# Kernel tuning notes

Measured on AMD Instinct MI355X. Metric: run time of the kernel, lower is better.

The kernel has to match this reference:

```python
import jax, jax.numpy as jnp
import numpy as np

H = 50  # hidden size hard-coded in the torch module


def _lstm_layer(x, W_ih, W_hh, b_ih, b_hh):
    """x: [B, T, D_in] -> outputs [B, T, H]. PyTorch gate order: i, f, g, o."""
    B = x.shape[0]
    # precompute input projection for all timesteps: [B, T, 4H]
    x_proj = jnp.einsum('btd,gd->btg', x, W_ih) + b_ih + b_hh
    x_proj = jnp.swapaxes(x_proj, 0, 1)  # time-major [T, B, 4H]

    def step(carry, xt):
        h, c = carry
        gates = xt + h @ W_hh.T  # [B, 4H]
        i, f, g, o = jnp.split(gates, 4, axis=-1)
        c = jax.nn.sigmoid(f) * c + jax.nn.sigmoid(i) * jnp.tanh(g)
        h = jax.nn.sigmoid(o) * jnp.tanh(c)
        return (h, c), h

    h0 = jnp.zeros((B, H), dtype=x.dtype)
    c0 = jnp.zeros((B, H), dtype=x.dtype)
    (_, _), hs = jax.lax.scan(step, (h0, c0), x_proj)
    return jnp.swapaxes(hs, 0, 1)  # [B, T, H]


def setup_inputs() -> dict:
    key = jax.random.key(0)
    ks = jax.random.split(key, 11)
    B, T = 4096, 512
    s = 1.0 / np.sqrt(H)  # torch LSTM init scale
    return {
        'x': jax.random.normal(ks[0], (B, T, 1), dtype=jnp.float32),
        'W_ih0': jax.random.normal(ks[1], (4 * H, 1), dtype=jnp.float32) * s,
        'W_hh0': jax.random.normal(ks[2], (4 * H, H), dtype=jnp.float32) * s,
        'b_ih0': jax.random.normal(ks[3], (4 * H,), dtype=jnp.float32) * s,
        'b_hh0': jax.random.normal(ks[4], (4 * H,), dtype=jnp.float32) * s,
        'W_ih1': jax.random.normal(ks[5], (4 * H, H), dtype=jnp.float32) * s,
        'W_hh1': jax.random.normal(ks[6], (4 * H, H), dtype=jnp.float32) * s,
        'b_ih1': jax.random.normal(ks[7], (4 * H,), dtype=jnp.float32) * s,
        'b_hh1': jax.random.normal(ks[8], (4 * H,), dtype=jnp.float32) * s,
        'W_fc': jax.random.normal(ks[9], (1, H), dtype=jnp.float32) * s,
        'b_fc': jax.random.normal(ks[10], (1,), dtype=jnp.float32) * s,
    }


def reference(x, W_ih0, W_hh0, b_ih0, b_hh0, W_ih1, W_hh1, b_ih1, b_hh1, W_fc, b_fc):
    h1 = _lstm_layer(x, W_ih0, W_hh0, b_ih0, b_hh0)   # [B, T, H]
    h2 = _lstm_layer(h1, W_ih1, W_hh1, b_ih1, b_hh1)  # [B, T, H]
    last = h2[:, -1, :]                                # [B, H]
    return last @ W_fc.T + b_fc                        # [B, 1]
```

## Files before the change

kernel.cpp:

```cpp
#include <hip/hip_runtime.h>


#define TT 512
#define HH 50
#define BT 16
#define NTHR 1024
#define L2E 1.44269504f

typedef _Float16 half8 __attribute__((ext_vector_type(8)));
typedef float floatx4 __attribute__((ext_vector_type(4)));

static __device__ __forceinline__ float fexp2(float x) { return __builtin_amdgcn_exp2f(x); }
static __device__ __forceinline__ float frcp(float x)  { return __builtin_amdgcn_rcpf(x); }

static __device__ __forceinline__ float cell_update(float gi, float gf, float gg,
                                                    float go, float& c) {
    float Ei = fexp2(gi);
    float Eg = fexp2(gg);
    float Ef = fexp2(gf);
    float Eo = fexp2(go);
    float p1 = (1.0f + Ei) * (1.0f + Eg);
    float fe = 1.0f + Ef;
    float R  = frcp(fe * p1);
    c = R * (c * p1 + (1.0f - Eg) * fe);
    float cl = fminf(fmaxf(c, -18.0f), 18.0f);
    float Ec = fexp2(cl * (-2.0f * L2E));
    float Ro = frcp((1.0f + Eo) * (1.0f + Ec));
    return (1.0f - Ec) * Ro;
}

#define MFMA(a, b, c) __builtin_amdgcn_mfma_f32_16x16x32_f16((a), (b), (c), 0, 0, 0)

template<int NJ, bool XW>
static __device__ __forceinline__ void run_l0(
    int tbase, int ln, _Float16 (*H1)[1024], const float* xs,
    const float* __restrict__ W_ih0, const float* __restrict__ W_hh0,
    const float* __restrict__ b_ih0, const float* __restrict__ b_hh0)
{
    const int m = ln & 15, q = ln >> 4;
    const float GSC[4] = { -L2E, -L2E, -2.0f * L2E, -L2E };

    half8 a0[NJ][2];
    float c[NJ];
    int   widx[NJ];
#pragma unroll
    for (int j = 0; j < NJ; ++j) {
        const int  tau  = tbase + j;
        const int  uA   = 4 * tau + (m >> 2);
        const int  gA   = m & 3;
        const bool rokA = (uA < HH);
        const int  wrow = gA * HH + uA;
        const float sA  = GSC[gA];
#pragma unroll
        for (int ks = 0; ks < 2; ++ks) {
            half8 h8;
#pragma unroll
            for (int jj = 0; jj < 8; ++jj) {
                int k = ks * 32 + q * 8 + jj;
                float w = 0.f;
                if (rokA) {
                    if (k < HH)       w = W_hh0[wrow * HH + k];
                    else if (k == 50) w = b_ih0[wrow] + b_hh0[wrow];
                    else if (k == 51) w = W_ih0[wrow];
                }
                h8[jj] = (_Float16)(sA * w);
            }
            a0[j][ks] = h8;
        }
        const int uC = 4 * tau + q;
        const int kh = (uC < HH) ? uC : (uC + 2);
        widx[j] = ((kh >> 5) * 64 + ((kh >> 3) & 3) * 16 + m) * 8 + (kh & 7);
        c[j] = 0.f;
    }

    __syncthreads();

    {
        const float xv = xs[m];
#pragma unroll
        for (int j = 0; j < NJ; ++j) {
            const int  uC = 4 * (tbase + j) + q;
            const bool vC = (uC < HH);
            float g4[4];
#pragma unroll
            for (int g = 0; g < 4; ++g) {
                int rg = g * HH + (vC ? uC : 0);
                g4[g] = vC ? GSC[g] * ((b_ih0[rg] + b_hh0[rg]) + W_ih0[rg] * xv) : 0.f;
            }
            float h = cell_update(g4[0], g4[1], g4[2], g4[3], c[j]);
            H1[0][widx[j]] = (_Float16)h;
        }
    }
    __syncthreads();

    const floatx4 ZERO = { 0.f, 0.f, 0.f, 0.f };
    for (int s = 1; s <= 513; ++s) {
        if (s <= 511) {
            const _Float16* bufR = H1[(s - 1) & 3];
            _Float16*       bufW = H1[s & 3];
            if (XW) {
                if (ln < 16)
                    bufW[(96 + ln) * 8 + 3] = (_Float16)xs[(s + 1) * BT + ln];
            }
            half8 b0 = *(const half8*)&bufR[(0  + ln) * 8];
            half8 b1 = *(const half8*)&bufR[(64 + ln) * 8];
#pragma unroll
            for (int j = 0; j < NJ; ++j) {
                floatx4 a = MFMA(a0[j][0], b0, ZERO);
                a = MFMA(a0[j][1], b1, a);
                float h = cell_update(a[0], a[1], a[2], a[3], c[j]);
                bufW[widx[j]] = (_Float16)h;
            }
        }
        __syncthreads();
    }
}

template<int NJ>
static __device__ __forceinline__ void run_l1(
    int tbase, int ln, _Float16 (*H1)[1024], _Float16 (*H2)[1024],
    const float* __restrict__ W_ih1, const float* __restrict__ W_hh1,
    const float* __restrict__ b_ih1, const float* __restrict__ b_hh1)
{
    const int m = ln & 15, q = ln >> 4;
    const float GSC[4] = { -L2E, -L2E, -2.0f * L2E, -L2E };

    half8 a1[NJ][4];
    float c[NJ];
    int   widx[NJ];
#pragma unroll
    for (int j = 0; j < NJ; ++j) {
        const int  tau  = tbase + j;
        const int  uA   = 4 * tau + (m >> 2);
        const int  gA   = m & 3;
        const bool rokA = (uA < HH);
        const int  wrow = gA * HH + uA;
        const float sA  = GSC[gA];
#pragma unroll
        for (int ks = 0; ks < 4; ++ks) {
            half8 h8;
#pragma unroll
            for (int jj = 0; jj < 8; ++jj) {
                int k = ks * 32 + q * 8 + jj;
                float w = 0.f;
                if (rokA) {
                    if (k < HH)                      w = W_ih1[wrow * HH + k];
                    else if (k == 50)                w = b_ih1[wrow] + b_hh1[wrow];
                    else if (k >= 64 && k < 64 + HH) w = W_hh1[wrow * HH + (k - 64)];
                }
                h8[jj] = (_Float16)(sA * w);
            }
            a1[j][ks] = h8;
        }
        const int uC = 4 * tau + q;
        const int kh = (uC < HH) ? uC : (uC + 2);
        widx[j] = ((kh >> 5) * 64 + ((kh >> 3) & 3) * 16 + m) * 8 + (kh & 7);
        c[j] = 0.f;
    }

    __syncthreads();
    __syncthreads();

    half8 p0 = {}, p1 = {};
    const floatx4 ZERO = { 0.f, 0.f, 0.f, 0.f };
    for (int s = 1; s <= 513; ++s) {
        if (s >= 2) {
            const _Float16* h2R = H2[(s - 1) & 1];
            _Float16*       h2W = H2[s & 1];
            half8 b2 = *(const half8*)&h2R[(0  + ln) * 8];
            half8 b3 = *(const half8*)&h2R[(64 + ln) * 8];
#pragma unroll
            for (int j = 0; j < NJ; ++j) {
                floatx4 a = MFMA(a1[j][0], p0, ZERO);
                a = MFMA(a1[j][1], p1, a);
                a = MFMA(a1[j][2], b2, a);
                a = MFMA(a1[j][3], b3, a);
                float h = cell_update(a[0], a[1], a[2], a[3], c[j]);
                h2W[widx[j]] = (_Float16)h;
            }
        }
        {
            const _Float16* h1R = H1[(s - 1) & 3];
            p0 = *(const half8*)&h1R[(0  + ln) * 8];
            p1 = *(const half8*)&h1R[(64 + ln) * 8];
        }
        __syncthreads();
    }
}

__global__ __launch_bounds__(NTHR, 4) void lstm_mfma(
    const float* __restrict__ x,
    const float* __restrict__ W_ih0, const float* __restrict__ W_hh0,
    const float* __restrict__ b_ih0, const float* __restrict__ b_hh0,
    const float* __restrict__ W_ih1, const float* __restrict__ W_hh1,
    const float* __restrict__ b_ih1, const float* __restrict__ b_hh1,
    const float* __restrict__ W_fc,  const float* __restrict__ b_fc,
    float* __restrict__ out)
{
    __shared__ __align__(16) _Float16 H1[4][1024];
    __shared__ __align__(16) _Float16 H2[2][1024];
    __shared__ float xs[(TT + 1) * BT];

    const int tid = threadIdx.x;
    const int ln  = tid & 63;
    const int wv  = tid >> 6;
    const int b0g = blockIdx.x * BT;

    for (int i = tid; i < BT * TT; i += NTHR) {
        int b = i & 15, t = i >> 4;
        xs[t * BT + b] = x[(size_t)(b0g + b) * TT + t];
    }
    if (tid < BT) xs[TT * BT + tid] = 0.f;
    for (int i = tid; i < 4 * 1024; i += NTHR) ((_Float16*)H1)[i] = (_Float16)0.f;
    for (int i = tid; i < 2 * 1024; i += NTHR) ((_Float16*)H2)[i] = (_Float16)0.f;
    __syncthreads();
    if (tid < 16) {
#pragma unroll
        for (int r = 0; r < 4; ++r) H1[r][(96 + tid) * 8 + 2] = (_Float16)1.0f;
        H1[0][(96 + tid) * 8 + 3] = (_Float16)xs[BT + tid];
    }

    if (wv < 8) {
        if (wv < 5)
            run_l0<2, false>(2 * wv, ln, H1, xs, W_ih0, W_hh0, b_ih0, b_hh0);
        else if (wv == 6)
            run_l0<1, true>(11, ln, H1, xs, W_ih0, W_hh0, b_ih0, b_hh0);
        else
            run_l0<1, false>(wv == 5 ? 10 : 12, ln, H1, xs,
                             W_ih0, W_hh0, b_ih0, b_hh0);
    } else {
        const int w = wv - 8;
        if (w < 3)
            run_l1<1>(w, ln, H1, H2, W_ih1, W_hh1, b_ih1, b_hh1);
        else
            run_l1<2>(3 + 2 * (w - 3), ln, H1, H2,
                      W_ih1, W_hh1, b_ih1, b_hh1);
    }

    if (tid < BT) {
        float a = b_fc[0];
        for (int u = 0; u < HH; ++u) {
            int idx = ((u >> 5) * 64 + ((u >> 3) & 3) * 16 + tid) * 8 + (u & 7);
            a = fmaf((float)H2[1][idx], W_fc[u], a);
        }
        out[b0g + tid] = a;
    }
}

extern "C" void kernel_launch(void* const* d_in, const int* in_sizes, int n_in,
                              void* d_out, int out_size, void* d_ws, size_t ws_size,
                              hipStream_t stream) {
    const float* x     = (const float*)d_in[0];
    const float* W_ih0 = (const float*)d_in[1];
    const float* W_hh0 = (const float*)d_in[2];
    const float* b_ih0 = (const float*)d_in[3];
    const float* b_hh0 = (const float*)d_in[4];
    const float* W_ih1 = (const float*)d_in[5];
    const float* W_hh1 = (const float*)d_in[6];
    const float* b_ih1 = (const float*)d_in[7];
    const float* b_hh1 = (const float*)d_in[8];
    const float* W_fc  = (const float*)d_in[9];
    const float* b_fc  = (const float*)d_in[10];
    float* out = (float*)d_out;

    dim3 grid(4096 / BT);
    dim3 block(NTHR);
    lstm_mfma<<<grid, block, 0, stream>>>(x, W_ih0, W_hh0, b_ih0, b_hh0,
                                          W_ih1, W_hh1, b_ih1, b_hh1,
                                          W_fc, b_fc, out);
}
```

Baseline: 363.7 us.

## Merge both LSTM layers into shared wavefronts with unified double-buffered state

Replaces the 16-wave split (8 waves for layer 0, 8 for layer 1) with 8 waves that each compute a mix of layer-0 and layer-1 unit groups. Both layers now read from one double-buffered shared state array, where layer 1 at step s consumes layer-0 h from step s-1, and waves on the critical path get raised priority. The intent is to halve the threads per block and barrier participants, balance MFMA and transcendental work per wave, and allow 2 blocks per CU. In exchange each wave carries more per-step work, occupancy changes, and the workload mapping (including a mixed tail tile) becomes harder to verify.

```diff
diff --git a/kernel.cpp b/kernel.cpp
--- a/kernel.cpp
+++ b/kernel.cpp
@@ -4,7 +4,7 @@
 #define TT 512
 #define HH 50
 #define BT 16
-#define NTHR 1024
+#define NTHR 512
 #define L2E 1.44269504f
 
 typedef _Float16 half8 __attribute__((ext_vector_type(8)));
@@ -31,164 +31,189 @@
 
 #define MFMA(a, b, c) __builtin_amdgcn_mfma_f32_16x16x32_f16((a), (b), (c), 0, 0, 0)
 
-template<int NJ, bool XW>
-static __device__ __forceinline__ void run_l0(
-    int tbase, int ln, _Float16 (*H1)[1024], const float* xs,
+static __device__ __forceinline__ int widx_of(int unit, int m) {
+    return ((unit >> 5) * 64 + ((unit >> 3) & 3) * 16 + m) * 8 + (unit & 7);
+}
+
+template<int NL0, int NL1, bool MX, bool XW, bool PRIO>
+static __device__ __forceinline__ void run(
+    int l0base, int l1base, int ln, _Float16 (*HS)[2048], const float* xs,
     const float* __restrict__ W_ih0, const float* __restrict__ W_hh0,
-    const float* __restrict__ b_ih0, const float* __restrict__ b_hh0)
-{
-    const int m = ln & 15, q = ln >> 4;
-    const float GSC[4] = { -L2E, -L2E, -2.0f * L2E, -L2E };
-
-    half8 a0[NJ][2];
-    float c[NJ];
-    int   widx[NJ];
-#pragma unroll
-    for (int j = 0; j < NJ; ++j) {
-        const int  tau  = tbase + j;
-        const int  uA   = 4 * tau + (m >> 2);
-        const int  gA   = m & 3;
-        const bool rokA = (uA < HH);
-        const int  wrow = gA * HH + uA;
-        const float sA  = GSC[gA];
-#pragma unroll
-        for (int ks = 0; ks < 2; ++ks) {
-            half8 h8;
-#pragma unroll
-            for (int jj = 0; jj < 8; ++jj) {
-                int k = ks * 32 + q * 8 + jj;
-                float w = 0.f;
-                if (rokA) {
-                    if (k < HH)       w = W_hh0[wrow * HH + k];
-                    else if (k == 50) w = b_ih0[wrow] + b_hh0[wrow];
-                    else if (k == 51) w = W_ih0[wrow];
-                }
-                h8[jj] = (_Float16)(sA * w);
-            }
-            a0[j][ks] = h8;
-        }
-        const int uC = 4 * tau + q;
-        const int kh = (uC < HH) ? uC : (uC + 2);
-        widx[j] = ((kh >> 5) * 64 + ((kh >> 3) & 3) * 16 + m) * 8 + (kh & 7);
-        c[j] = 0.f;
-    }
-
-    __syncthreads();
-
-    {
-        const float xv = xs[m];
-#pragma unroll
-        for (int j = 0; j < NJ; ++j) {
-            const int  uC = 4 * (tbase + j) + q;
-            const bool vC = (uC < HH);
-            float g4[4];
-#pragma unroll
-            for (int g = 0; g < 4; ++g) {
-                int rg = g * HH + (vC ? uC : 0);
-                g4[g] = vC ? GSC[g] * ((b_ih0[rg] + b_hh0[rg]) + W_ih0[rg] * xv) : 0.f;
-            }
-            float h = cell_update(g4[0], g4[1], g4[2], g4[3], c[j]);
-            H1[0][widx[j]] = (_Float16)h;
-        }
-    }
-    __syncthreads();
-
-    const floatx4 ZERO = { 0.f, 0.f, 0.f, 0.f };
-    for (int s = 1; s <= 513; ++s) {
-        if (s <= 511) {
-            const _Float16* bufR = H1[(s - 1) & 3];
-            _Float16*       bufW = H1[s & 3];
-            if (XW) {
-                if (ln < 16)
-                    bufW[(96 + ln) * 8 + 3] = (_Float16)xs[(s + 1) * BT + ln];
-            }
-            half8 b0 = *(const half8*)&bufR[(0  + ln) * 8];
-            half8 b1 = *(const half8*)&bufR[(64 + ln) * 8];
-#pragma unroll
-            for (int j = 0; j < NJ; ++j) {
-                floatx4 a = MFMA(a0[j][0], b0, ZERO);
-                a = MFMA(a0[j][1], b1, a);
-                float h = cell_update(a[0], a[1], a[2], a[3], c[j]);
-                bufW[widx[j]] = (_Float16)h;
-            }
-        }
-        __syncthreads();
-    }
-}
-
-template<int NJ>
-static __device__ __forceinline__ void run_l1(
-    int tbase, int ln, _Float16 (*H1)[1024], _Float16 (*H2)[1024],
+    const float* __restrict__ b_ih0, const float* __restrict__ b_hh0,
     const float* __restrict__ W_ih1, const float* __restrict__ W_hh1,
     const float* __restrict__ b_ih1, const float* __restrict__ b_hh1)
 {
     const int m = ln & 15, q = ln >> 4;
     const float GSC[4] = { -L2E, -L2E, -2.0f * L2E, -L2E };
-
-    half8 a1[NJ][4];
-    float c[NJ];
-    int   widx[NJ];
-#pragma unroll
-    for (int j = 0; j < NJ; ++j) {
-        const int  tau  = tbase + j;
-        const int  uA   = 4 * tau + (m >> 2);
-        const int  gA   = m & 3;
-        const bool rokA = (uA < HH);
-        const int  wrow = gA * HH + uA;
-        const float sA  = GSC[gA];
-#pragma unroll
-        for (int ks = 0; ks < 4; ++ks) {
+    const int  gA = m & 3;
+    const float sA = GSC[gA];
+
+    half8 a0[NL0 ? NL0 : 1][2];
+    float c0[NL0 ? NL0 : 1];
+    int   w0i[NL0 ? NL0 : 1];
+#pragma unroll
+    for (int j = 0; j < NL0; ++j) {
+        const int uA = 4 * (l0base + j) + (m >> 2);
+        const int wrow = gA * HH + uA;
+#pragma unroll
+        for (int ks = 0; ks < 2; ++ks) {
             half8 h8;
 #pragma unroll
             for (int jj = 0; jj < 8; ++jj) {
                 int k = ks * 32 + q * 8 + jj;
                 float w = 0.f;
-                if (rokA) {
+                if (k < HH)       w = W_hh0[wrow * HH + k];
+                else if (k == 50) w = b_ih0[wrow] + b_hh0[wrow];
+                else if (k == 51) w = W_ih0[wrow];
+                h8[jj] = (_Float16)(sA * w);
+            }
+            a0[j][ks] = h8;
+        }
+        w0i[j] = widx_of(4 * (l0base + j) + q, m);
+        c0[j] = 0.f;
+    }
+
+    half8 a1[NL1 ? NL1 : 1][4];
+    float c1[NL1 ? NL1 : 1];
+    int   w1i[NL1 ? NL1 : 1];
+#pragma unroll
+    for (int j = 0; j < NL1; ++j) {
+        const int uA = 4 * (l1base + j) + (m >> 2);
+        const int wrow = gA * HH + uA;
+#pragma unroll
+        for (int ks = 0; ks < 4; ++ks) {
+            half8 h8;
+#pragma unroll
+            for (int jj = 0; jj < 8; ++jj) {
+                int k = ks * 32 + q * 8 + jj;
+                float w = 0.f;
+                if (k < HH)                      w = W_ih1[wrow * HH + k];
+                else if (k == 50)                w = b_ih1[wrow] + b_hh1[wrow];
+                else if (k >= 64 && k < 64 + HH) w = W_hh1[wrow * HH + (k - 64)];
+                h8[jj] = (_Float16)(sA * w);
+            }
+            a1[j][ks] = h8;
+        }
+        w1i[j] = 1024 + widx_of(4 * (l1base + j) + q, m);
+        c1[j] = 0.f;
+    }
+
+    half8 amx[4];
+    float cmx = 0.f;
+    int   wmxi = 0;
+    if (MX) {
+        const int sel  = m >> 2;
+        const bool lo  = (sel < 2);
+        const int unit = lo ? (48 + sel) : (46 + sel);
+        const int wrow = gA * HH + unit;
+#pragma unroll
+        for (int ks = 0; ks < 4; ++ks) {
+            half8 h8;
+#pragma unroll
+            for (int jj = 0; jj < 8; ++jj) {
+                int k = ks * 32 + q * 8 + jj;
+                float w = 0.f;
+                if (lo) {
+                    if (k < HH)       w = W_hh0[wrow * HH + k];
+                    else if (k == 50) w = b_ih0[wrow] + b_hh0[wrow];
+                    else if (k == 51) w = W_ih0[wrow];
+                } else {
                     if (k < HH)                      w = W_ih1[wrow * HH + k];
                     else if (k == 50)                w = b_ih1[wrow] + b_hh1[wrow];
                     else if (k >= 64 && k < 64 + HH) w = W_hh1[wrow * HH + (k - 64)];
                 }
                 h8[jj] = (_Float16)(sA * w);
             }
-            a1[j][ks] = h8;
-        }
-        const int uC = 4 * tau + q;
-        const int kh = (uC < HH) ? uC : (uC + 2);
-        widx[j] = ((kh >> 5) * 64 + ((kh >> 3) & 3) * 16 + m) * 8 + (kh & 7);
-        c[j] = 0.f;
-    }
-
+            amx[ks] = h8;
+        }
+        const int cu = (q < 2) ? (48 + q) : (46 + q);
+        wmxi = ((q < 2) ? 0 : 1024) + widx_of(cu, m);
+    }
+
+    if (PRIO) __builtin_amdgcn_s_setprio(1);
+
+    {
+        const float xv = xs[m];
+#pragma unroll
+        for (int j = 0; j < NL0; ++j) {
+            const int uC = 4 * (l0base + j) + q;
+            float g4[4];
+#pragma unroll
+            for (int g = 0; g < 4; ++g) {
+                int rg = g * HH + uC;
+                g4[g] = GSC[g] * ((b_ih0[rg] + b_hh0[rg]) + W_ih0[rg] * xv);
+            }
+            float h = cell_update(g4[0], g4[1], g4[2], g4[3], c0[j]);
+            HS[0][w0i[j]] = (_Float16)h;
+        }
+        if (MX) {
+            if (q < 2) {
+                const int uC = 48 + q;
+                float g4[4];
+#pragma unroll
+                for (int g = 0; g < 4; ++g) {
+                    int rg = g * HH + uC;
+                    g4[g] = GSC[g] * ((b_ih0[rg] + b_hh0[rg]) + W_ih0[rg] * xv);
+                }
+                float h = cell_update(g4[0], g4[1], g4[2], g4[3], cmx);
+                HS[0][wmxi] = (_Float16)h;
+            }
+        }
+    }
     __syncthreads();
-    __syncthreads();
-
-    half8 p0 = {}, p1 = {};
+
     const floatx4 ZERO = { 0.f, 0.f, 0.f, 0.f };
-    for (int s = 1; s <= 513; ++s) {
-        if (s >= 2) {
-            const _Float16* h2R = H2[(s - 1) & 1];
-            _Float16*       h2W = H2[s & 1];
-            half8 b2 = *(const half8*)&h2R[(0  + ln) * 8];
-            half8 b3 = *(const half8*)&h2R[(64 + ln) * 8];
-#pragma unroll
-            for (int j = 0; j < NJ; ++j) {
-                floatx4 a = MFMA(a1[j][0], p0, ZERO);
-                a = MFMA(a1[j][1], p1, a);
-                a = MFMA(a1[j][2], b2, a);
-                a = MFMA(a1[j][3], b3, a);
-                float h = cell_update(a[0], a[1], a[2], a[3], c[j]);
-                h2W[widx[j]] = (_Float16)h;
-            }
-        }
-        {
-            const _Float16* h1R = H1[(s - 1) & 3];
-            p0 = *(const half8*)&h1R[(0  + ln) * 8];
-            p1 = *(const half8*)&h1R[(64 + ln) * 8];
-        }
-        __syncthreads();
-    }
-}
-
-__global__ __launch_bounds__(NTHR, 4) void lstm_mfma(
+
+#define STEP(P, S)                                                          \
+    {                                                                       \
+        const _Float16* Rb = HS[(P)];                                       \
+        _Float16*       Wb = HS[(P) ^ 1];                                   \
+        if (XW) {                                                           \
+            if (ln < 16)                                                    \
+                Wb[(96 + ln) * 8 + 3] = (_Float16)xs[((S) + 1) * BT + ln];  \
+        }                                                                   \
+        half8 b0 = *(const half8*)&Rb[(0   + ln) * 8];                      \
+        half8 b1 = *(const half8*)&Rb[(64  + ln) * 8];                      \
+        half8 b2, b3;                                                       \
+        if (NL1 > 0 || MX) {                                                \
+            b2 = *(const half8*)&Rb[(128 + ln) * 8];                        \
+            b3 = *(const half8*)&Rb[(192 + ln) * 8];                        \
+        }                                                                   \
+        _Pragma("unroll")                                                   \
+        for (int j = 0; j < NL0; ++j) {                                     \
+            floatx4 a = MFMA(a0[j][0], b0, ZERO);                           \
+            a = MFMA(a0[j][1], b1, a);                                      \
+            float h = cell_update(a[0], a[1], a[2], a[3], c0[j]);           \
+            Wb[w0i[j]] = (_Float16)h;                                       \
+        }                                                                   \
+        _Pragma("unroll")                                                   \
+        for (int j = 0; j < NL1; ++j) {                                     \
+            floatx4 a = MFMA(a1[j][0], b0, ZERO);                           \
+            a = MFMA(a1[j][1], b1, a);                                      \
+            a = MFMA(a1[j][2], b2, a);                                      \
+            a = MFMA(a1[j][3], b3, a);                                      \
+            float h = cell_update(a[0], a[1], a[2], a[3], c1[j]);           \
+            Wb[w1i[j]] = (_Float16)h;                                       \
+        }                                                                   \
+        if (MX) {                                                           \
+            floatx4 a = MFMA(amx[0], b0, ZERO);                             \
+            a = MFMA(amx[1], b1, a);                                        \
+            a = MFMA(amx[2], b2, a);                                        \
+            a = MFMA(amx[3], b3, a);                                        \
+            float h = cell_update(a[0], a[1], a[2], a[3], cmx);             \
+            Wb[wmxi] = (_Float16)h;                                         \
+        }                                                                   \
+        __syncthreads();                                                    \
+    }
+
+    for (int k = 0; k < 256; ++k) {
+        STEP(0, 2 * k + 1);
+        STEP(1, 2 * k + 2);
+    }
+#undef STEP
+}
+
+__global__ __launch_bounds__(NTHR, 2) void lstm_mfma(
     const float* __restrict__ x,
     const float* __restrict__ W_ih0, const float* __restrict__ W_hh0,
     const float* __restrict__ b_ih0, const float* __restrict__ b_hh0,
@@ -197,9 +222,8 @@
     const float* __restrict__ W_fc,  const float* __restrict__ b_fc,
     float* __restrict__ out)
 {
-    __shared__ __align__(16) _Float16 H1[4][1024];
-    __shared__ __align__(16) _Float16 H2[2][1024];
-    __shared__ float xs[(TT + 1) * BT];
+    __shared__ __align__(16) _Float16 HS[2][2048];
+    __shared__ float xs[(TT + 2) * BT];
 
     const int tid = threadIdx.x;
     const int ln  = tid & 63;
@@ -210,38 +234,31 @@
         int b = i & 15, t = i >> 4;
         xs[t * BT + b] = x[(size_t)(b0g + b) * TT + t];
     }
-    if (tid < BT) xs[TT * BT + tid] = 0.f;
-    for (int i = tid; i < 4 * 1024; i += NTHR) ((_Float16*)H1)[i] = (_Float16)0.f;
-    for (int i = tid; i < 2 * 1024; i += NTHR) ((_Float16*)H2)[i] = (_Float16)0.f;
+    if (tid < 2 * BT) xs[TT * BT + tid] = 0.f;
+    for (int i = tid; i < 2 * 2048; i += NTHR) ((_Float16*)HS)[i] = (_Float16)0.f;
     __syncthreads();
     if (tid < 16) {
-#pragma unroll
-        for (int r = 0; r < 4; ++r) H1[r][(96 + tid) * 8 + 2] = (_Float16)1.0f;
-        H1[0][(96 + tid) * 8 + 3] = (_Float16)xs[BT + tid];
-    }
-
-    if (wv < 8) {
-        if (wv < 5)
-            run_l0<2, false>(2 * wv, ln, H1, xs, W_ih0, W_hh0, b_ih0, b_hh0);
-        else if (wv == 6)
-            run_l0<1, true>(11, ln, H1, xs, W_ih0, W_hh0, b_ih0, b_hh0);
-        else
-            run_l0<1, false>(wv == 5 ? 10 : 12, ln, H1, xs,
-                             W_ih0, W_hh0, b_ih0, b_hh0);
-    } else {
-        const int w = wv - 8;
-        if (w < 3)
-            run_l1<1>(w, ln, H1, H2, W_ih1, W_hh1, b_ih1, b_hh1);
-        else
-            run_l1<2>(3 + 2 * (w - 3), ln, H1, H2,
-                      W_ih1, W_hh1, b_ih1, b_hh1);
+        HS[0][(96 + tid) * 8 + 2] = (_Float16)1.0f;
+        HS[1][(96 + tid) * 8 + 2] = (_Float16)1.0f;
+        HS[0][(96 + tid) * 8 + 3] = (_Float16)xs[BT + tid];
+    }
+
+    switch (wv) {
+    case 0: run<4, 0, false, false, true >(0,  0, ln, HS, xs, W_ih0, W_hh0, b_ih0, b_hh0, W_ih1, W_hh1, b_ih1, b_hh1); break;
+    case 1: run<2, 1, false, true,  false>(4,  0, ln, HS, xs, W_ih0, W_hh0, b_ih0, b_hh0, W_ih1, W_hh1, b_ih1, b_hh1); break;
+    case 2: run<2, 1, false, false, false>(6,  1, ln, HS, xs, W_ih0, W_hh0, b_ih0, b_hh0, W_ih1, W_hh1, b_ih1, b_hh1); break;
+    case 3: run<2, 1, false, false, false>(8,  2, ln, HS, xs, W_ih0, W_hh0, b_ih0, b_hh0, W_ih1, W_hh1, b_ih1, b_hh1); break;
+    case 4: run<0, 3, false, false, true >(0,  3, ln, HS, xs, W_ih0, W_hh0, b_ih0, b_hh0, W_ih1, W_hh1, b_ih1, b_hh1); break;
+    case 5: run<1, 2, false, false, false>(10, 6, ln, HS, xs, W_ih0, W_hh0, b_ih0, b_hh0, W_ih1, W_hh1, b_ih1, b_hh1); break;
+    case 6: run<1, 2, false, false, false>(11, 8, ln, HS, xs, W_ih0, W_hh0, b_ih0, b_hh0, W_ih1, W_hh1, b_ih1, b_hh1); break;
+    default: run<0, 2, true, false, false>(0, 10, ln, HS, xs, W_ih0, W_hh0, b_ih0, b_hh0, W_ih1, W_hh1, b_ih1, b_hh1); break;
     }
 
     if (tid < BT) {
         float a = b_fc[0];
         for (int u = 0; u < HH; ++u) {
-            int idx = ((u >> 5) * 64 + ((u >> 3) & 3) * 16 + tid) * 8 + (u & 7);
-            a = fmaf((float)H2[1][idx], W_fc[u], a);
+            int idx = 1024 + ((u >> 5) * 64 + ((u >> 3) & 3) * 16 + tid) * 8 + (u & 7);
+            a = fmaf((float)HS[0][idx], W_fc[u], a);
         }
         out[b0g + tid] = a;
     }
```

New measurement: 350.2 us, median of 2. -3.7%, faster.
